# Kernel tuning notes

Measured on AMD Instinct MI355X. Metric: run time of the kernel, lower is better.

## Reference

```python
import jax, jax.numpy as jnp
import numpy as np

DIM = 512
HEADS = 8
D_HEAD = 64
INNER = HEADS * D_HEAD  # 512
CTX_DIM = 768
FF_INNER = 4 * DIM  # 2048
SCALE = D_HEAD ** -0.5
LN_EPS = 1e-5


def layer_norm(x, g, b):
    mu = jnp.mean(x, axis=-1, keepdims=True)
    var = jnp.var(x, axis=-1, keepdims=True)
    return (x - mu) * jax.lax.rsqrt(var + LN_EPS) * g + b


def attention(x, ctx, qw, kw, vw, ow, ob):
    B, N, _ = x.shape
    M = ctx.shape[1]
    q = (x @ qw).reshape(B, N, HEADS, D_HEAD).transpose(0, 2, 1, 3)
    k = (ctx @ kw).reshape(B, M, HEADS, D_HEAD).transpose(0, 2, 1, 3)
    v = (ctx @ vw).reshape(B, M, HEADS, D_HEAD).transpose(0, 2, 1, 3)
    sim = jnp.einsum('bhid,bhjd->bhij', q, k) * SCALE  # [B,H,N,M]
    attn = jax.nn.softmax(sim, axis=-1)
    out = jnp.einsum('bhij,bhjd->bhid', attn, v)
    out = out.transpose(0, 2, 1, 3).reshape(B, N, INNER)
    return out @ ow + ob


def setup_inputs() -> dict:
    key = jax.random.key(0)
    ks = jax.random.split(key, 20)
    r = lambda k, shp, s=0.02: jax.random.normal(k, shp, dtype=jnp.float32) * s
    return {
        'x': jax.random.normal(ks[0], (2, 4096, DIM), dtype=jnp.float32),
        'context': jax.random.normal(ks[1], (2, 256, CTX_DIM), dtype=jnp.float32),
        'q1_w': r(ks[2], (DIM, INNER)), 'k1_w': r(ks[3], (DIM, INNER)),
        'v1_w': r(ks[4], (DIM, INNER)), 'o1_w': r(ks[5], (INNER, DIM)),
        'o1_b': jnp.zeros((DIM,), jnp.float32),
        'q2_w': r(ks[6], (DIM, INNER)), 'k2_w': r(ks[7], (CTX_DIM, INNER)),
        'v2_w': r(ks[8], (CTX_DIM, INNER)), 'o2_w': r(ks[9], (INNER, DIM)),
        'o2_b': jnp.zeros((DIM,), jnp.float32),
        'ff_in_w': r(ks[10], (DIM, 2 * FF_INNER)), 'ff_in_b': jnp.zeros((2 * FF_INNER,), jnp.float32),
        'ff_out_w': r(ks[11], (FF_INNER, DIM)), 'ff_out_b': jnp.zeros((DIM,), jnp.float32),
        'ln1_g': jnp.ones((DIM,), jnp.float32), 'ln1_b': jnp.zeros((DIM,), jnp.float32),
        'ln2_g': jnp.ones((DIM,), jnp.float32), 'ln2_b': jnp.zeros((DIM,), jnp.float32),
        'ln3_g': jnp.ones((DIM,), jnp.float32), 'ln3_b': jnp.zeros((DIM,), jnp.float32),
    }


def reference(x, context, q1_w, k1_w, v1_w, o1_w, o1_b,
              q2_w, k2_w, v2_w, o2_w, o2_b,
              ff_in_w, ff_in_b, ff_out_w, ff_out_b,
              ln1_g, ln1_b, ln2_g, ln2_b, ln3_g, ln3_b):
    # self-attention + residual
    h = layer_norm(x, ln1_g, ln1_b)
    x = attention(h, h, q1_w, k1_w, v1_w, o1_w, o1_b) + x
    # cross-attention + residual
    h = layer_norm(x, ln2_g, ln2_b)
    x = attention(h, context, q2_w, k2_w, v2_w, o2_w, o2_b) + x
    # GEGLU feed-forward + residual (torch F.gelu is exact erf form)
    h = layer_norm(x, ln3_g, ln3_b)
    proj = h @ ff_in_w + ff_in_b
    val, gate = jnp.split(proj, 2, axis=-1)
    ff = (val * jax.nn.gelu(gate, approximate=False)) @ ff_out_w + ff_out_b
    return ff + x
```

## Files before the change

### kernel.cpp

```cpp
#include <hip/hip_runtime.h>
#include <hip/hip_bf16.h>
#include <cstdint>


typedef __bf16 bf16_t;
typedef __bf16 bf16x8 __attribute__((ext_vector_type(8)));
typedef float f32x4 __attribute__((ext_vector_type(4)));
typedef float f32x16 __attribute__((ext_vector_type(16)));

__device__ __forceinline__ bf16_t f2bf(float f) { return (bf16_t)f; }

__device__ __forceinline__ f32x4 mfma16(bf16x8 a, bf16x8 b, f32x4 c) {
  return __builtin_amdgcn_mfma_f32_16x16x32_bf16(a, b, c, 0, 0, 0);
}
__device__ __forceinline__ f32x16 mfma32(bf16x8 a, bf16x8 b, f32x16 c) {
  return __builtin_amdgcn_mfma_f32_32x32x16_bf16(a, b, c, 0, 0, 0);
}

__device__ __forceinline__ float gelu_exact(float x) {
  return 0.5f * x * (1.0f + erff(x * 0.70710678118654752f));
}

__device__ __forceinline__ void gload_lds16(const bf16_t* g, bf16_t* lds) {
  __builtin_amdgcn_global_load_lds(
      (const __attribute__((address_space(1))) unsigned int*)g,
      (__attribute__((address_space(3))) unsigned int*)lds, 16, 0, 0);
}

__global__ __launch_bounds__(256) void ln_kernel(const float* __restrict__ in,
                                                 const float* __restrict__ gw,
                                                 const float* __restrict__ bw,
                                                 bf16_t* __restrict__ out) {
  int w = threadIdx.x >> 6, l = threadIdx.x & 63;
  size_t row = (size_t)blockIdx.x * 4 + w;
  const float* p = in + row * 512 + l * 8;
  f32x4 va = *(const f32x4*)p;
  f32x4 vb = *(const f32x4*)(p + 4);
  float xs[8] = {va[0], va[1], va[2], va[3], vb[0], vb[1], vb[2], vb[3]};
  float s = 0.f;
#pragma unroll
  for (int j = 0; j < 8; j++) s += xs[j];
#pragma unroll
  for (int m = 1; m < 64; m <<= 1) s += __shfl_xor(s, m);
  float mu = s * (1.0f / 512.0f);
  float v = 0.f;
#pragma unroll
  for (int j = 0; j < 8; j++) { float d = xs[j] - mu; v += d * d; }
#pragma unroll
  for (int m = 1; m < 64; m <<= 1) v += __shfl_xor(v, m);
  float rstd = rsqrtf(v * (1.0f / 512.0f) + 1e-5f);
  f32x4 g0 = *(const f32x4*)(gw + l * 8);
  f32x4 g1 = *(const f32x4*)(gw + l * 8 + 4);
  f32x4 b0 = *(const f32x4*)(bw + l * 8);
  f32x4 b1 = *(const f32x4*)(bw + l * 8 + 4);
  bf16x8 o;
#pragma unroll
  for (int j = 0; j < 4; j++) o[j] = f2bf((xs[j] - mu) * rstd * g0[j] + b0[j]);
#pragma unroll
  for (int j = 0; j < 4; j++) o[4 + j] = f2bf((xs[4 + j] - mu) * rstd * g1[j] + b1[j]);
  *(bf16x8*)(out + row * 512 + l * 8) = o;
}

struct WJob {
  const float* W;
  bf16_t* Wt;
  int K;
  int N;
  float sc;
  int tile0;
};
struct WJobs {
  WJob j[10];
};

__global__ __launch_bounds__(256) void wtrans_all_kernel(WJobs jobs) {
  __shared__ float t[32][33];
  int bid = blockIdx.x;
  int i = 0;
#pragma unroll
  for (int q = 1; q < 10; q++)
    if (bid >= jobs.j[q].tile0) i = q;
  WJob jb = jobs.j[i];
  int tt = bid - jb.tile0;
  int ktiles = jb.K >> 5;
  int k0 = (tt % ktiles) * 32, n0 = (tt / ktiles) * 32;
#pragma unroll
  for (int s = 0; s < 4; s++) {
    int idx = threadIdx.x + s * 256;
    int kk = idx >> 5, nn = idx & 31;
    t[kk][nn] = jb.W[(size_t)(k0 + kk) * jb.N + n0 + nn];
  }
  __syncthreads();
#pragma unroll
  for (int s = 0; s < 4; s++) {
    int idx = threadIdx.x + s * 256;
    int nn = idx >> 5, kk = idx & 31;
    jb.Wt[(size_t)(n0 + nn) * jb.K + k0 + kk] = f2bf(t[kk][nn] * jb.sc);
  }
}

__global__ __launch_bounds__(256) void cvt_kernel(const float* __restrict__ in,
                                                  bf16_t* __restrict__ out) {
  int i = (blockIdx.x * 256 + threadIdx.x) * 4;
  f32x4 v = *(const f32x4*)(in + i);
  out[i + 0] = f2bf(v[0]);
  out[i + 1] = f2bf(v[1]);
  out[i + 2] = f2bf(v[2]);
  out[i + 3] = f2bf(v[3]);
}

template <int BM, int BN, int EPI>
__global__ __launch_bounds__(256) void gemm_kernel(
    const bf16_t* __restrict__ A, const bf16_t* __restrict__ Bt,
    const float* __restrict__ bias, const float* __restrict__ res,
    void* __restrict__ outp, int M, int N, int K, int gateOff, int ldo) {
  constexpr int WR = BM / 2;
  constexpr int WN = BN / 2;
  constexpr int MF = WR / 16;
  constexpr int NF = WN / 16;
  constexpr int ABLK = BM / 64;
  constexpr int BROWS = (EPI == 2) ? 2 * BN : BN;
  constexpr int BBLK = BROWS / 64;
  __shared__ bf16_t Al[2][2][BM][32];
  __shared__ bf16_t Bl[2][2][BROWS][32];

  int tid = threadIdx.x;
  int w = tid >> 6, l = tid & 63;
  int wr = w >> 1, wc = w & 1;
  int lg = l >> 4, lc = l & 15;
  int m0 = blockIdx.x * BM, n0 = blockIdx.y * BN;

  f32x4 acc[MF][NF] = {};
  f32x4 acc2[MF][NF] = {};

  int srow = tid >> 2, scol = (tid & 3) * 8;
  const bf16_t* aP[ABLK];
#pragma unroll
  for (int i = 0; i < ABLK; i++)
    aP[i] = A + (size_t)(m0 + i * 64 + srow) * K + scol;
  const bf16_t* bP[BBLK];
  if (EPI == 2) {
    bP[0] = Bt + (size_t)(n0 + srow) * K + scol;
    bP[1] = Bt + (size_t)(n0 + gateOff + srow) * K + scol;
  } else {
#pragma unroll
    for (int i = 0; i < BBLK; i++)
      bP[i] = Bt + (size_t)(n0 + i * 64 + srow) * K + scol;
  }

  auto STAGE = [&](int buf, int k0) {
#pragma unroll
    for (int kh = 0; kh < 2; kh++) {
#pragma unroll
      for (int i = 0; i < ABLK; i++)
        gload_lds16(aP[i] + k0 + kh * 32, &Al[buf][kh][i * 64 + w * 16][0]);
#pragma unroll
      for (int i = 0; i < BBLK; i++)
        gload_lds16(bP[i] + k0 + kh * 32, &Bl[buf][kh][i * 64 + w * 16][0]);
    }
  };

  int nk = K / 64;
  int cur = 0;
  STAGE(0, 0);
  __syncthreads();

  for (int t = 0; t < nk; ++t) {
    if (t + 1 < nk) STAGE(cur ^ 1, (t + 1) * 64);

#pragma unroll
    for (int kh = 0; kh < 2; kh++) {
      bf16x8 af[MF];
#pragma unroll
      for (int mi = 0; mi < MF; mi++)
        af[mi] = *(const bf16x8*)&Al[cur][kh][wr * WR + mi * 16 + lc][lg * 8];
      bf16x8 bfr[NF];
#pragma unroll
      for (int ni = 0; ni < NF; ni++)
        bfr[ni] = *(const bf16x8*)&Bl[cur][kh][wc * WN + ni * 16 + lc][lg * 8];
#pragma unroll
      for (int mi = 0; mi < MF; mi++)
#pragma unroll
        for (int ni = 0; ni < NF; ni++)
          acc[mi][ni] = mfma16(af[mi], bfr[ni], acc[mi][ni]);
      if (EPI == 2) {
        bf16x8 bg[NF];
#pragma unroll
        for (int ni = 0; ni < NF; ni++)
          bg[ni] =
              *(const bf16x8*)&Bl[cur][kh][BN + wc * WN + ni * 16 + lc][lg * 8];
#pragma unroll
        for (int mi = 0; mi < MF; mi++)
#pragma unroll
          for (int ni = 0; ni < NF; ni++)
            acc2[mi][ni] = mfma16(af[mi], bg[ni], acc2[mi][ni]);
      }
    }
    __syncthreads();
    cur ^= 1;
  }

#pragma unroll
  for (int mi = 0; mi < MF; mi++) {
#pragma unroll
    for (int ni = 0; ni < NF; ni++) {
#pragma unroll
      for (int r = 0; r < 4; r++) {
        int row = m0 + wr * WR + mi * 16 + lg * 4 + r;
        int col = n0 + wc * WN + ni * 16 + lc;
        float v = acc[mi][ni][r];
        if (EPI == 0) {
          ((bf16_t*)outp)[(size_t)row * ldo + col] = f2bf(v);
        } else if (EPI == 3) {
          int cs = (col & ~15) | (lc & 3) | ((lc & 4) << 1) | ((lc & 8) >> 1);
          ((bf16_t*)outp)[(size_t)row * ldo + cs] = f2bf(v);
        } else if (EPI == 1) {
          ((float*)outp)[(size_t)row * ldo + col] =
              v + bias[col] + res[(size_t)row * ldo + col];
        } else {
          float g = acc2[mi][ni][r] + bias[col + gateOff];
          float val = v + bias[col];
          ((bf16_t*)outp)[(size_t)row * ldo + col] = f2bf(val * gelu_exact(g));
        }
      }
    }
  }
}

__global__ __launch_bounds__(256) void cross_fused_kernel(
    const bf16_t* __restrict__ hb, const bf16_t* __restrict__ q2t,
    bf16_t* __restrict__ qkb, const bf16_t* __restrict__ ctxb,
    const bf16_t* __restrict__ k2t, bf16_t* __restrict__ kb,
    const bf16_t* __restrict__ v2t, bf16_t* __restrict__ vtg2) {
  constexpr int BM = 64, BN = 128;
  constexpr int WR = 32, WN = 64, MF = 2, NF = 4;
  __shared__ bf16_t Al[2][2][BM][32];
  __shared__ bf16_t Bl[2][2][BN][32];

  const bf16_t* A;
  const bf16_t* Bt;
  bf16_t* outp;
  int K, m0;
  bool perm = false;
  if (blockIdx.z == 0) {
    A = hb; Bt = q2t; outp = qkb; K = 512; m0 = blockIdx.x * BM;
  } else {
    int bx = blockIdx.x;
    if (bx >= 16) return;
    K = 768;
    if (bx < 8) {
      A = ctxb; Bt = k2t; outp = kb; m0 = bx * BM;
    } else {
      A = v2t; Bt = ctxb; outp = vtg2; perm = true; m0 = (bx - 8) * BM;
    }
  }
  const int ldo = 512;
  int n0 = blockIdx.y * BN;

  int tid = threadIdx.x;
  int w = tid >> 6, l = tid & 63;
  int wr = w >> 1, wc = w & 1;
  int lg = l >> 4, lc = l & 15;

  f32x4 acc[MF][NF] = {};

  int srow = tid >> 2, scol = (tid & 3) * 8;
  const bf16_t* aP0 = A + (size_t)(m0 + srow) * K + scol;
  const bf16_t* bP0 = Bt + (size_t)(n0 + srow) * K + scol;
  const bf16_t* bP1 = Bt + (size_t)(n0 + 64 + srow) * K + scol;

  auto STAGE = [&](int buf, int k0) {
#pragma unroll
    for (int kh = 0; kh < 2; kh++) {
      gload_lds16(aP0 + k0 + kh * 32, &Al[buf][kh][w * 16][0]);
      gload_lds16(bP0 + k0 + kh * 32, &Bl[buf][kh][w * 16][0]);
      gload_lds16(bP1 + k0 + kh * 32, &Bl[buf][kh][64 + w * 16][0]);
    }
  };

  int nk = K / 64;
  int cur = 0;
  STAGE(0, 0);
  __syncthreads();

  for (int t = 0; t < nk; ++t) {
    if (t + 1 < nk) STAGE(cur ^ 1, (t + 1) * 64);
#pragma unroll
    for (int kh = 0; kh < 2; kh++) {
      bf16x8 af[MF];
#pragma unroll
      for (int mi = 0; mi < MF; mi++)
        af[mi] = *(const bf16x8*)&Al[cur][kh][wr * WR + mi * 16 + lc][lg * 8];
      bf16x8 bfr[NF];
#pragma unroll
      for (int ni = 0; ni < NF; ni++)
        bfr[ni] = *(const bf16x8*)&Bl[cur][kh][wc * WN + ni * 16 + lc][lg * 8];
#pragma unroll
      for (int mi = 0; mi < MF; mi++)
#pragma unroll
        for (int ni = 0; ni < NF; ni++)
          acc[mi][ni] = mfma16(af[mi], bfr[ni], acc[mi][ni]);
    }
    __syncthreads();
    cur ^= 1;
  }

#pragma unroll
  for (int mi = 0; mi < MF; mi++) {
#pragma unroll
    for (int ni = 0; ni < NF; ni++) {
#pragma unroll
      for (int r = 0; r < 4; r++) {
        int row = m0 + wr * WR + mi * 16 + lg * 4 + r;
        int col = n0 + wc * WN + ni * 16 + lc;
        int cs = perm ? ((col & ~15) | (lc & 3) | ((lc & 4) << 1) |
                         ((lc & 8) >> 1))
                      : col;
        outp[(size_t)row * ldo + cs] = f2bf(acc[mi][ni][r]);
      }
    }
  }
}

__global__ __launch_bounds__(256) void attn_kernel(
    const bf16_t* __restrict__ Q, int ldq, const bf16_t* __restrict__ Kb,
    int ldk, const bf16_t* __restrict__ Vt, bf16_t* __restrict__ O, int Mkv) {
  __shared__ bf16_t Klds[64][72];
  __shared__ bf16_t Vlds[64][72];

  int lin = blockIdx.x;
  int xcd = lin & 7, slot = lin >> 3;
  int pair = 2 * xcd + (slot >> 5);
  int qt = slot & 31;
  int head = pair & 7, b = pair >> 3;

  int tid = threadIdx.x;
  int w = tid >> 6, l = tid & 63;
  int ql = l & 31, hi = l >> 5;
  int ldv = 2 * Mkv;

  size_t qrow = (size_t)b * 4096 + qt * 128 + w * 32 + ql;
  const bf16_t* qp = Q + qrow * ldq + head * 64 + hi * 8;
  bf16x8 qf[4];
#pragma unroll
  for (int dk = 0; dk < 4; dk++) qf[dk] = *(const bf16x8*)(qp + dk * 16);

  f32x16 o0 = {}, o1 = {};
  f32x16 zacc = {};
  float mrun = -1e30f;

  bf16x8 vones;
#pragma unroll
  for (int j = 0; j < 8; j++) vones[j] = f2bf(1.0f);

  int key0 = tid >> 2, dc0 = (tid & 3) * 16;
  const bf16_t* kp = Kb + ((size_t)b * Mkv + key0) * ldk + head * 64 + dc0;
  const bf16_t* vp = Vt + (size_t)(head * 64 + key0) * ldv + b * Mkv + dc0;

  bf16x8 kc0 = *(const bf16x8*)kp, kc1 = *(const bf16x8*)(kp + 8);
  bf16x8 vc0 = *(const bf16x8*)vp, vc1 = *(const bf16x8*)(vp + 8);

  for (int t0 = 0; t0 < Mkv; t0 += 64) {
    __syncthreads();
    *(bf16x8*)&Klds[key0][dc0] = kc0;
    *(bf16x8*)&Klds[key0][dc0 + 8] = kc1;
    *(bf16x8*)&Vlds[key0][dc0] = vc0;
    *(bf16x8*)&Vlds[key0][dc0 + 8] = vc1;
    __syncthreads();

    if (t0 + 64 < Mkv) {
      kp += (size_t)64 * ldk;
      vp += 64;
      kc0 = *(const bf16x8*)kp;
      kc1 = *(const bf16x8*)(kp + 8);
      vc0 = *(const bf16x8*)vp;
      vc1 = *(const bf16x8*)(vp + 8);
    }

    f32x16 s0 = {}, s1 = {};
    __builtin_amdgcn_s_setprio(1);
#pragma unroll
    for (int dk = 0; dk < 4; dk++) {
      bf16x8 a0 = *(const bf16x8*)&Klds[ql][dk * 16 + hi * 8];
      bf16x8 a1 = *(const bf16x8*)&Klds[32 + ql][dk * 16 + hi * 8];
      s0 = mfma32(a0, qf[dk], s0);
      s1 = mfma32(a1, qf[dk], s1);
    }
    __builtin_amdgcn_s_setprio(0);

    float tmax = s0[0];
#pragma unroll
    for (int r = 1; r < 16; r++) tmax = fmaxf(tmax, s0[r]);
#pragma unroll
    for (int r = 0; r < 16; r++) tmax = fmaxf(tmax, s1[r]);
    tmax = fmaxf(tmax, __shfl_xor(tmax, 32));

    if (!__all(tmax <= mrun + 8.0f)) {
      float mnew = fmaxf(mrun, tmax);
      float resc = __builtin_amdgcn_exp2f(mrun - mnew);
      mrun = mnew;
#pragma unroll
      for (int r = 0; r < 16; r++) {
        float f = __shfl(resc, (r & 3) + 8 * (r >> 2) + 4 * hi);
        o0[r] *= f;
        o1[r] *= f;
        zacc[r] *= f;
      }
    }

    bf16x8 pa[4];
#pragma unroll
    for (int m = 0; m < 4; m++) {
#pragma unroll
      for (int j = 0; j < 8; j++) {
        float sv = (m < 2) ? s0[(m & 1) * 8 + j] : s1[(m & 1) * 8 + j];
        pa[m][j] = f2bf(__builtin_amdgcn_exp2f(sv - mrun));
      }
    }

    __builtin_amdgcn_s_setprio(1);
#pragma unroll
    for (int m = 0; m < 4; m++) {
      zacc = mfma32(pa[m], vones, zacc);
      bf16x8 vb0 = *(const bf16x8*)&Vlds[ql][m * 16 + hi * 8];
      bf16x8 vb1 = *(const bf16x8*)&Vlds[32 + ql][m * 16 + hi * 8];
      o0 = mfma32(pa[m], vb0, o0);
      o1 = mfma32(pa[m], vb1, o1);
    }
    __builtin_amdgcn_s_setprio(0);
  }

  size_t ob = ((size_t)b * 4096 + qt * 128 + w * 32) * 512 + head * 64;
#pragma unroll
  for (int r = 0; r < 16; r++) {
    float inv = 1.0f / zacc[r];
    int q = (r & 3) + 8 * (r >> 2) + 4 * hi;
    O[ob + (size_t)q * 512 + ql] = f2bf(o0[r] * inv);
    O[ob + (size_t)q * 512 + 32 + ql] = f2bf(o1[r] * inv);
  }
}

extern "C" void kernel_launch(void* const* d_in, const int* in_sizes, int n_in,
                              void* d_out, int out_size, void* d_ws,
                              size_t ws_size, hipStream_t stream) {
  const float* x = (const float*)d_in[0];
  const float* ctx = (const float*)d_in[1];
  const float* q1_w = (const float*)d_in[2];
  const float* k1_w = (const float*)d_in[3];
  const float* v1_w = (const float*)d_in[4];
  const float* o1_w = (const float*)d_in[5];
  const float* o1_b = (const float*)d_in[6];
  const float* q2_w = (const float*)d_in[7];
  const float* k2_w = (const float*)d_in[8];
  const float* v2_w = (const float*)d_in[9];
  const float* o2_w = (const float*)d_in[10];
  const float* o2_b = (const float*)d_in[11];
  const float* ff_in_w = (const float*)d_in[12];
  const float* ff_in_b = (const float*)d_in[13];
  const float* ff_out_w = (const float*)d_in[14];
  const float* ff_out_b = (const float*)d_in[15];
  const float* ln1_g = (const float*)d_in[16];
  const float* ln1_b = (const float*)d_in[17];
  const float* ln2_g = (const float*)d_in[18];
  const float* ln2_b = (const float*)d_in[19];
  const float* ln3_g = (const float*)d_in[20];
  const float* ln3_b = (const float*)d_in[21];

  char* ws = (char*)d_ws;
  float* xr = (float*)(ws + 0);
  bf16_t* hb = (bf16_t*)(ws + 16777216);
  bf16_t* qkb = (bf16_t*)(ws + 25165824);
  bf16_t* ao = (bf16_t*)(ws + 41943040);
  bf16_t* ffmid = qkb;
  bf16_t* kb = (bf16_t*)(ws + 50331648);
  bf16_t* vtg2 = (bf16_t*)(ws + 50855936);
  bf16_t* ctxb = (bf16_t*)(ws + 51380224);
  bf16_t* wts = (bf16_t*)(ws + 58720256);
  bf16_t* vtg = (bf16_t*)(ws + 69730304);

  bf16_t* q1t = wts + 0;
  bf16_t* k1t = wts + 262144;
  bf16_t* v1t = wts + 524288;
  bf16_t* o1t = wts + 786432;
  bf16_t* q2t = wts + 1048576;
  bf16_t* k2t = wts + 1310720;
  bf16_t* v2t = wts + 1703936;
  bf16_t* o2t = wts + 2097152;
  bf16_t* ffint = wts + 2359296;
  bf16_t* ffoutt = wts + 4456448;

  const float QS = 0.125f * 1.44269504f;

  WJobs jobs;
  auto setj = [&](int i, const float* W, bf16_t* Wt, int K, int N, float sc,
                  int tile0) {
    jobs.j[i] = WJob{W, Wt, K, N, sc, tile0};
  };
  setj(0, q1_w, q1t, 512, 512, QS, 0);
  setj(1, k1_w, k1t, 512, 512, 1.0f, 256);
  setj(2, v1_w, v1t, 512, 512, 1.0f, 512);
  setj(3, o1_w, o1t, 512, 512, 1.0f, 768);
  setj(4, q2_w, q2t, 512, 512, QS, 1024);
  setj(5, k2_w, k2t, 768, 512, 1.0f, 1280);
  setj(6, v2_w, v2t, 768, 512, 1.0f, 1664);
  setj(7, o2_w, o2t, 512, 512, 1.0f, 2048);
  setj(8, ff_in_w, ffint, 512, 4096, 1.0f, 2304);
  setj(9, ff_out_w, ffoutt, 2048, 512, 1.0f, 4352);
  wtrans_all_kernel<<<5376, 256, 0, stream>>>(jobs);
  cvt_kernel<<<384, 256, 0, stream>>>(ctx, ctxb);

  ln_kernel<<<2048, 256, 0, stream>>>(x, ln1_g, ln1_b, hb);
  gemm_kernel<128, 128, 0><<<dim3(64, 8), 256, 0, stream>>>(
      hb, q1t, nullptr, nullptr, qkb, 8192, 1024, 512, 0, 1024);
  gemm_kernel<64, 128, 3><<<dim3(8, 64), 256, 0, stream>>>(
      v1t, hb, nullptr, nullptr, vtg, 512, 8192, 512, 0, 8192);
  attn_kernel<<<512, 256, 0, stream>>>(qkb, 1024, qkb + 512, 1024, vtg, ao,
                                       4096);
  gemm_kernel<64, 128, 1><<<dim3(128, 4), 256, 0, stream>>>(
      ao, o1t, o1_b, x, xr, 8192, 512, 512, 0, 512);

  ln_kernel<<<2048, 256, 0, stream>>>(xr, ln2_g, ln2_b, hb);
  cross_fused_kernel<<<dim3(128, 4, 2), 256, 0, stream>>>(
      hb, q2t, qkb, ctxb, k2t, kb, v2t, vtg2);
  attn_kernel<<<512, 256, 0, stream>>>(qkb, 512, kb, 512, vtg2, ao, 256);
  gemm_kernel<64, 128, 1><<<dim3(128, 4), 256, 0, stream>>>(
      ao, o2t, o2_b, xr, xr, 8192, 512, 512, 0, 512);

  ln_kernel<<<2048, 256, 0, stream>>>(xr, ln3_g, ln3_b, hb);
  gemm_kernel<128, 64, 2><<<dim3(64, 32), 256, 0, stream>>>(
      hb, ffint, ff_in_b, nullptr, ffmid, 8192, 2048, 512, 2048, 2048);
  gemm_kernel<64, 128, 1><<<dim3(128, 4), 256, 0, stream>>>(
      ffmid, ffoutt, ff_out_b, xr, (float*)d_out, 8192, 512, 2048, 0, 512);
}
```

Before: 290.2 us.

## Double-buffer attention K/V tiles and swizzle GEMM block order across XCDs

The attention kernel now keeps two LDS buffers for K and V. The next tile is written into the spare buffer after the current tile's compute, which cuts the two barriers per iteration down to one. The GEMM kernel remaps its linear block index so that consecutive blocks dispatched to the same XCD cover adjacent tiles, aiming for better L2 reuse. The changes cost double the LDS in attention, which may lower occupancy, and the remap assumes the grid size is divisible by 8.

```diff
diff --git a/kernel.cpp b/kernel.cpp
--- a/kernel.cpp
+++ b/kernel.cpp
@@ -128,7 +128,12 @@
   int w = tid >> 6, l = tid & 63;
   int wr = w >> 1, wc = w & 1;
   int lg = l >> 4, lc = l & 15;
-  int m0 = blockIdx.x * BM, n0 = blockIdx.y * BN;
+
+  int ntiles = gridDim.y;
+  int lin = blockIdx.y * gridDim.x + blockIdx.x;
+  int cpx = (gridDim.x * gridDim.y) >> 3;
+  int v = (lin & 7) * cpx + (lin >> 3);
+  int m0 = (v / ntiles) * BM, n0 = (v % ntiles) * BN;
 
   f32x4 acc[MF][NF] = {};
   f32x4 acc2[MF][NF] = {};
@@ -208,18 +213,18 @@
       for (int r = 0; r < 4; r++) {
         int row = m0 + wr * WR + mi * 16 + lg * 4 + r;
         int col = n0 + wc * WN + ni * 16 + lc;
-        float v = acc[mi][ni][r];
+        float v2 = acc[mi][ni][r];
         if (EPI == 0) {
-          ((bf16_t*)outp)[(size_t)row * ldo + col] = f2bf(v);
+          ((bf16_t*)outp)[(size_t)row * ldo + col] = f2bf(v2);
         } else if (EPI == 3) {
           int cs = (col & ~15) | (lc & 3) | ((lc & 4) << 1) | ((lc & 8) >> 1);
-          ((bf16_t*)outp)[(size_t)row * ldo + cs] = f2bf(v);
+          ((bf16_t*)outp)[(size_t)row * ldo + cs] = f2bf(v2);
         } else if (EPI == 1) {
           ((float*)outp)[(size_t)row * ldo + col] =
-              v + bias[col] + res[(size_t)row * ldo + col];
+              v2 + bias[col] + res[(size_t)row * ldo + col];
         } else {
           float g = acc2[mi][ni][r] + bias[col + gateOff];
-          float val = v + bias[col];
+          float val = v2 + bias[col];
           ((bf16_t*)outp)[(size_t)row * ldo + col] = f2bf(val * gelu_exact(g));
         }
       }
@@ -325,8 +330,8 @@
 __global__ __launch_bounds__(256) void attn_kernel(
     const bf16_t* __restrict__ Q, int ldq, const bf16_t* __restrict__ Kb,
     int ldk, const bf16_t* __restrict__ Vt, bf16_t* __restrict__ O, int Mkv) {
-  __shared__ bf16_t Klds[64][72];
-  __shared__ bf16_t Vlds[64][72];
+  __shared__ bf16_t Klds[2][64][72];
+  __shared__ bf16_t Vlds[2][64][72];
 
   int lin = blockIdx.x;
   int xcd = lin & 7, slot = lin >> 3;
@@ -357,32 +362,33 @@
   const bf16_t* kp = Kb + ((size_t)b * Mkv + key0) * ldk + head * 64 + dc0;
   const bf16_t* vp = Vt + (size_t)(head * 64 + key0) * ldv + b * Mkv + dc0;
 
+  int nt = Mkv / 64;
+
   bf16x8 kc0 = *(const bf16x8*)kp, kc1 = *(const bf16x8*)(kp + 8);
   bf16x8 vc0 = *(const bf16x8*)vp, vc1 = *(const bf16x8*)(vp + 8);
-
-  for (int t0 = 0; t0 < Mkv; t0 += 64) {
-    __syncthreads();
-    *(bf16x8*)&Klds[key0][dc0] = kc0;
-    *(bf16x8*)&Klds[key0][dc0 + 8] = kc1;
-    *(bf16x8*)&Vlds[key0][dc0] = vc0;
-    *(bf16x8*)&Vlds[key0][dc0 + 8] = vc1;
-    __syncthreads();
-
-    if (t0 + 64 < Mkv) {
-      kp += (size_t)64 * ldk;
-      vp += 64;
-      kc0 = *(const bf16x8*)kp;
-      kc1 = *(const bf16x8*)(kp + 8);
-      vc0 = *(const bf16x8*)vp;
-      vc1 = *(const bf16x8*)(vp + 8);
-    }
+  *(bf16x8*)&Klds[0][key0][dc0] = kc0;
+  *(bf16x8*)&Klds[0][key0][dc0 + 8] = kc1;
+  *(bf16x8*)&Vlds[0][key0][dc0] = vc0;
+  *(bf16x8*)&Vlds[0][key0][dc0 + 8] = vc1;
+  if (nt > 1) {
+    kp += (size_t)64 * ldk;
+    vp += 64;
+    kc0 = *(const bf16x8*)kp;
+    kc1 = *(const bf16x8*)(kp + 8);
+    vc0 = *(const bf16x8*)vp;
+    vc1 = *(const bf16x8*)(vp + 8);
+  }
+  __syncthreads();
+
+  for (int t = 0; t < nt; ++t) {
+    int cur = t & 1;
 
     f32x16 s0 = {}, s1 = {};
     __builtin_amdgcn_s_setprio(1);
 #pragma unroll
     for (int dk = 0; dk < 4; dk++) {
-      bf16x8 a0 = *(const bf16x8*)&Klds[ql][dk * 16 + hi * 8];
-      bf16x8 a1 = *(const bf16x8*)&Klds[32 + ql][dk * 16 + hi * 8];
+      bf16x8 a0 = *(const bf16x8*)&Klds[cur][ql][dk * 16 + hi * 8];
+      bf16x8 a1 = *(const bf16x8*)&Klds[cur][32 + ql][dk * 16 + hi * 8];
       s0 = mfma32(a0, qf[dk], s0);
       s1 = mfma32(a1, qf[dk], s1);
     }
@@ -422,12 +428,28 @@
 #pragma unroll
     for (int m = 0; m < 4; m++) {
       zacc = mfma32(pa[m], vones, zacc);
-      bf16x8 vb0 = *(const bf16x8*)&Vlds[ql][m * 16 + hi * 8];
-      bf16x8 vb1 = *(const bf16x8*)&Vlds[32 + ql][m * 16 + hi * 8];
+      bf16x8 vb0 = *(const bf16x8*)&Vlds[cur][ql][m * 16 + hi * 8];
+      bf16x8 vb1 = *(const bf16x8*)&Vlds[cur][32 + ql][m * 16 + hi * 8];
       o0 = mfma32(pa[m], vb0, o0);
       o1 = mfma32(pa[m], vb1, o1);
     }
     __builtin_amdgcn_s_setprio(0);
+
+    if (t + 1 < nt) {
+      *(bf16x8*)&Klds[cur ^ 1][key0][dc0] = kc0;
+      *(bf16x8*)&Klds[cur ^ 1][key0][dc0 + 8] = kc1;
+      *(bf16x8*)&Vlds[cur ^ 1][key0][dc0] = vc0;
+      *(bf16x8*)&Vlds[cur ^ 1][key0][dc0 + 8] = vc1;
+      if (t + 2 < nt) {
+        kp += (size_t)64 * ldk;
+        vp += 64;
+        kc0 = *(const bf16x8*)kp;
+        kc1 = *(const bf16x8*)(kp + 8);
+        vc0 = *(const bf16x8*)vp;
+        vc1 = *(const bf16x8*)(vp + 8);
+      }
+      __syncthreads();
+    }
   }
 
   size_t ob = ((size_t)b * 4096 + qt * 128 + w * 32) * 512 + head * 64;
```

Measured after the change: 282.7 us. 2.6% less time.
